# Kernel tuning notes

Hardware: AMD Instinct MI355X
Metric: run time of the kernel (lower is better)

Reference implementation:

```python
import jax, jax.numpy as jnp
import numpy as np

N_NODES = 100000
N_EDGES = 1600000
D_FEAT = 64
ORDER = 2


def setup_inputs() -> dict:
    key = jax.random.key(0)
    k1, k2, k3, k4 = jax.random.split(key, 4)
    x = jax.random.normal(k1, (N_NODES, D_FEAT), dtype=jnp.float32)
    edge_row = jnp.sort(jax.random.randint(k2, (N_EDGES,), 0, N_NODES, dtype=jnp.int32))
    edge_col = jax.random.randint(k3, (N_EDGES,), 0, N_NODES, dtype=jnp.int32)
    # positive edge weights ~ normalized adjacency values
    edge_val = jax.random.uniform(k4, (N_EDGES,), dtype=jnp.float32)
    return {"x": x, "edge_row": edge_row, "edge_col": edge_col, "edge_val": edge_val}


def reference(x, edge_row, edge_col, edge_val):
    # SGConvolution: x <- adj @ x, repeated `order` times (no trainable params).
    # adj is sparse COO: adj[edge_row[e], edge_col[e]] = edge_val[e].
    def spmm(h):
        # gather source features, scale by edge weight, scatter-add to rows
        msg = edge_val[:, None] * h[edge_col]          # [E, D]
        return jax.ops.segment_sum(msg, edge_row, num_segments=N_NODES)  # [N, D]

    h = x
    for _ in range(ORDER):
        h = spmm(h)
    return h
```

## Files before the change

kernel.cpp:

```cpp
#include <hip/hip_runtime.h>
#include <hip/hip_fp16.h>


#define N_NODES 100000
#define N_EDGES 1600000
#define D_FEAT  64
#define EPW     64
#define CH      16

__device__ __forceinline__ float readlane_f(float x, int j) {
    return __uint_as_float(__builtin_amdgcn_readlane(__float_as_uint(x), j));
}

__device__ __forceinline__ float to_f32(float x)  { return x; }
__device__ __forceinline__ float to_f32(__half x) { return __half2float(x); }

template <typename GT>
__global__ __launch_bounds__(256) void sg_spmm(
    const GT*    __restrict__ h,
    const int*   __restrict__ erow,
    const int*   __restrict__ ecol,
    const float* __restrict__ eval,
    float*       __restrict__ out)
{
    const int lane  = threadIdx.x & 63;
    const int wave  = (int)((blockIdx.x * blockDim.x + threadIdx.x) >> 6);
    const int start = wave * EPW;

    const int   r_v = erow[start + lane];
    const int   c_v = ecol[start + lane];
    const float w_v = eval[start + lane];

    GT gbuf[2][CH];

#pragma unroll
    for (int j = 0; j < CH; ++j) {
        const int c = __builtin_amdgcn_readlane(c_v, j);
        gbuf[0][j] = h[(size_t)c * D_FEAT + lane];
    }

    int   cur_row = __builtin_amdgcn_readlane(r_v, 0);
    float acc     = 0.0f;

#pragma unroll
    for (int k = 0; k < EPW / CH; ++k) {
        if (k + 1 < EPW / CH) {
#pragma unroll
            for (int j = 0; j < CH; ++j) {
                const int c = __builtin_amdgcn_readlane(c_v, (k + 1) * CH + j);
                gbuf[(k + 1) & 1][j] = h[(size_t)c * D_FEAT + lane];
            }
        }
#pragma unroll
        for (int j = 0; j < CH; ++j) {
            const int e = k * CH + j;
            const int r = __builtin_amdgcn_readlane(r_v, e);
            if (r != cur_row) {
                atomicAdd(&out[(size_t)cur_row * D_FEAT + lane], acc);
                acc = 0.0f;
                cur_row = r;
            }
            acc += readlane_f(w_v, e) * to_f32(gbuf[k & 1][j]);
        }
    }
    atomicAdd(&out[(size_t)cur_row * D_FEAT + lane], acc);
}

__global__ __launch_bounds__(256) void cast_f32_to_f16(
    const float* __restrict__ in, __half* __restrict__ out, int n4)
{
    const int i = blockIdx.x * blockDim.x + threadIdx.x;
    if (i >= n4) return;
    const float4 v = ((const float4*)in)[i];
    __half2 a = __floats2half2_rn(v.x, v.y);
    __half2 b = __floats2half2_rn(v.z, v.w);
    ((__half2*)out)[2 * i]     = a;
    ((__half2*)out)[2 * i + 1] = b;
}

extern "C" void kernel_launch(void* const* d_in, const int* in_sizes, int n_in,
                              void* d_out, int out_size, void* d_ws, size_t ws_size,
                              hipStream_t stream) {
    const float* x    = (const float*)d_in[0];
    const int*   erow = (const int*)  d_in[1];
    const int*   ecol = (const int*)  d_in[2];
    const float* eval = (const float*)d_in[3];
    float*       out  = (float*)d_out;

    const size_t n_elem     = (size_t)N_NODES * D_FEAT;
    const size_t f32_bytes  = n_elem * sizeof(float);
    const size_t f16_bytes  = n_elem * sizeof(__half);

    float*  h1f32 = (float*)d_ws;
    __half* h16   = (__half*)((char*)d_ws + f32_bytes);

    const int threads = 256;
    const int spmm_blocks = (N_EDGES / EPW) * 64 / threads;
    const int n4          = (int)(n_elem / 4);
    const int cast_blocks = (n4 + threads - 1) / threads;

    hipMemsetAsync(h1f32, 0, f32_bytes, stream);
    hipMemsetAsync(out,   0, f32_bytes, stream);

    if (ws_size >= f32_bytes + f16_bytes) {
        cast_f32_to_f16<<<cast_blocks, threads, 0, stream>>>(x, h16, n4);
        sg_spmm<__half><<<spmm_blocks, threads, 0, stream>>>(h16, erow, ecol, eval, h1f32);
        cast_f32_to_f16<<<cast_blocks, threads, 0, stream>>>(h1f32, h16, n4);
        sg_spmm<__half><<<spmm_blocks, threads, 0, stream>>>(h16, erow, ecol, eval, out);
    } else {
        sg_spmm<float><<<spmm_blocks, threads, 0, stream>>>(x, erow, ecol, eval, h1f32);
        sg_spmm<float><<<spmm_blocks, threads, 0, stream>>>(h1f32, erow, ecol, eval, out);
    }
}
```

Before: 170.1 us.

## Fuse prep into one kernel and accumulate first SpMM directly in fp16

One prep kernel now does the input cast to fp16 and zeroes both the intermediate buffer and the output, replacing two memsets and a cast launch. The first SpMM flushes its row partials as packed half2 atomics straight into an fp16 intermediate, which removes the fp32 intermediate and the second cast kernel. Atomic traffic for that stage is halved. In exchange the intermediate sum is accumulated in half precision through many atomics, so rounding error grows, and the fallback path for a small workspace is gone.

```diff
diff --git a/kernel.cpp b/kernel.cpp
--- a/kernel.cpp
+++ b/kernel.cpp
@@ -8,20 +8,37 @@
 #define EPW     64
 #define CH      16
 
+#define N_ELEM   (N_NODES * D_FEAT)
+#define N_CAST   (N_ELEM / 4)
+#define N_Z16    (N_ELEM / 8)
+#define N_ZOUT   (N_ELEM / 4)
+#define PREP_TASKS (N_CAST + N_Z16 + N_ZOUT)
+
 __device__ __forceinline__ float readlane_f(float x, int j) {
     return __uint_as_float(__builtin_amdgcn_readlane(__float_as_uint(x), j));
 }
 
-__device__ __forceinline__ float to_f32(float x)  { return x; }
-__device__ __forceinline__ float to_f32(__half x) { return __half2float(x); }
+template <bool HALF_OUT>
+__device__ __forceinline__ void flush(void* outp, int row, int lane, float acc) {
+    if constexpr (HALF_OUT) {
+        const float partner = __shfl_xor(acc, 1);
+        if ((lane & 1) == 0) {
+            __half2* o = (__half2*)outp;
+            unsafeAtomicAdd(&o[(size_t)row * (D_FEAT / 2) + (lane >> 1)],
+                            __floats2half2_rn(acc, partner));
+        }
+    } else {
+        atomicAdd(&((float*)outp)[(size_t)row * D_FEAT + lane], acc);
+    }
+}
 
-template <typename GT>
+template <bool HALF_OUT>
 __global__ __launch_bounds__(256) void sg_spmm(
-    const GT*    __restrict__ h,
-    const int*   __restrict__ erow,
-    const int*   __restrict__ ecol,
-    const float* __restrict__ eval,
-    float*       __restrict__ out)
+    const __half* __restrict__ h,
+    const int*    __restrict__ erow,
+    const int*    __restrict__ ecol,
+    const float*  __restrict__ eval,
+    void*         __restrict__ outp)
 {
     const int lane  = threadIdx.x & 63;
     const int wave  = (int)((blockIdx.x * blockDim.x + threadIdx.x) >> 6);
@@ -31,7 +48,7 @@
     const int   c_v = ecol[start + lane];
     const float w_v = eval[start + lane];
 
-    GT gbuf[2][CH];
+    __half gbuf[2][CH];
 
 #pragma unroll
     for (int j = 0; j < CH; ++j) {
@@ -56,26 +73,36 @@
             const int e = k * CH + j;
             const int r = __builtin_amdgcn_readlane(r_v, e);
             if (r != cur_row) {
-                atomicAdd(&out[(size_t)cur_row * D_FEAT + lane], acc);
+                flush<HALF_OUT>(outp, cur_row, lane, acc);
                 acc = 0.0f;
                 cur_row = r;
             }
-            acc += readlane_f(w_v, e) * to_f32(gbuf[k & 1][j]);
+            acc += readlane_f(w_v, e) * __half2float(gbuf[k & 1][j]);
         }
     }
-    atomicAdd(&out[(size_t)cur_row * D_FEAT + lane], acc);
+    flush<HALF_OUT>(outp, cur_row, lane, acc);
 }
 
-__global__ __launch_bounds__(256) void cast_f32_to_f16(
-    const float* __restrict__ in, __half* __restrict__ out, int n4)
+__global__ __launch_bounds__(256) void prep(
+    const float* __restrict__ x,
+    __half*      __restrict__ h16a,
+    __half*      __restrict__ h16b,
+    float*       __restrict__ out)
 {
     const int i = blockIdx.x * blockDim.x + threadIdx.x;
-    if (i >= n4) return;
-    const float4 v = ((const float4*)in)[i];
-    __half2 a = __floats2half2_rn(v.x, v.y);
-    __half2 b = __floats2half2_rn(v.z, v.w);
-    ((__half2*)out)[2 * i]     = a;
-    ((__half2*)out)[2 * i + 1] = b;
+    if (i < N_CAST) {
+        const float4 v = ((const float4*)x)[i];
+        const __half2 a = __floats2half2_rn(v.x, v.y);
+        const __half2 b = __floats2half2_rn(v.z, v.w);
+        uint2 u;
+        u.x = *(const unsigned int*)&a;
+        u.y = *(const unsigned int*)&b;
+        ((uint2*)h16a)[i] = u;
+    } else if (i < N_CAST + N_Z16) {
+        ((uint4*)h16b)[i - N_CAST] = make_uint4(0u, 0u, 0u, 0u);
+    } else {
+        ((float4*)out)[i - (N_CAST + N_Z16)] = make_float4(0.f, 0.f, 0.f, 0.f);
+    }
 }
 
 extern "C" void kernel_launch(void* const* d_in, const int* in_sizes, int n_in,
@@ -87,28 +114,14 @@
     const float* eval = (const float*)d_in[3];
     float*       out  = (float*)d_out;
 
-    const size_t n_elem     = (size_t)N_NODES * D_FEAT;
-    const size_t f32_bytes  = n_elem * sizeof(float);
-    const size_t f16_bytes  = n_elem * sizeof(__half);
+    __half* h16a = (__half*)d_ws;
+    __half* h16b = h16a + N_ELEM;
 
-    float*  h1f32 = (float*)d_ws;
-    __half* h16   = (__half*)((char*)d_ws + f32_bytes);
+    const int threads     = 256;
+    const int prep_blocks = PREP_TASKS / threads;
+    const int spmm_blocks = (N_EDGES / EPW) * 64 / threads;
 
-    const int threads = 256;
-    const int spmm_blocks = (N_EDGES / EPW) * 64 / threads;
-    const int n4          = (int)(n_elem / 4);
-    const int cast_blocks = (n4 + threads - 1) / threads;
-
-    hipMemsetAsync(h1f32, 0, f32_bytes, stream);
-    hipMemsetAsync(out,   0, f32_bytes, stream);
-
-    if (ws_size >= f32_bytes + f16_bytes) {
-        cast_f32_to_f16<<<cast_blocks, threads, 0, stream>>>(x, h16, n4);
-        sg_spmm<__half><<<spmm_blocks, threads, 0, stream>>>(h16, erow, ecol, eval, h1f32);
-        cast_f32_to_f16<<<cast_blocks, threads, 0, stream>>>(h1f32, h16, n4);
-        sg_spmm<__half><<<spmm_blocks, threads, 0, stream>>>(h16, erow, ecol, eval, out);
-    } else {
-        sg_spmm<float><<<spmm_blocks, threads, 0, stream>>>(x, erow, ecol, eval, h1f32);
-        sg_spmm<float><<<spmm_blocks, threads, 0, stream>>>(h1f32, erow, ecol, eval, out);
-    }
+    prep<<<prep_blocks, threads, 0, stream>>>(x, h16a, h16b, out);
+    sg_spmm<true ><<<spmm_blocks, threads, 0, stream>>>(h16a, erow, ecol, eval, h16b);
+    sg_spmm<false><<<spmm_blocks, threads, 0, stream>>>(h16b, erow, ecol, eval, out);
 }
```

Measured after the change: 153.9 us. -9.5%, faster.

## Fuse fp16 casts into SpMM by accumulating intermediate with half2 atomics

Applied to the files above, without the earlier changes.

The first SpMM pass now reads fp32 input directly and accumulates into an fp16 intermediate using packed half2 atomics. The second pass gathers that fp16 buffer and writes fp32 output. This removes both cast kernels, the fp32 intermediate buffer and one memset. In exchange, the first pass gathers fp32 rows and accumulates in fp16 atomics, which reduces precision. The output buffer is no longer zeroed before atomics accumulate into it.

```diff
diff --git a/kernel.cpp b/kernel.cpp
--- a/kernel.cpp
+++ b/kernel.cpp
@@ -8,6 +8,8 @@
 #define EPW     64
 #define CH      16
 
+#define N_ELEM  (N_NODES * D_FEAT)
+
 __device__ __forceinline__ float readlane_f(float x, int j) {
     return __uint_as_float(__builtin_amdgcn_readlane(__float_as_uint(x), j));
 }
@@ -15,13 +17,27 @@
 __device__ __forceinline__ float to_f32(float x)  { return x; }
 __device__ __forceinline__ float to_f32(__half x) { return __half2float(x); }
 
-template <typename GT>
+template <bool HALF_OUT>
+__device__ __forceinline__ void flush(void* outp, int row, int lane, float acc) {
+    if constexpr (HALF_OUT) {
+        const float partner = __shfl_xor(acc, 1);
+        if ((lane & 1) == 0) {
+            __half2* o = (__half2*)outp;
+            unsafeAtomicAdd(&o[(size_t)row * (D_FEAT / 2) + (lane >> 1)],
+                            __floats2half2_rn(acc, partner));
+        }
+    } else {
+        atomicAdd(&((float*)outp)[(size_t)row * D_FEAT + lane], acc);
+    }
+}
+
+template <typename GT, bool HALF_OUT>
 __global__ __launch_bounds__(256) void sg_spmm(
     const GT*    __restrict__ h,
     const int*   __restrict__ erow,
     const int*   __restrict__ ecol,
     const float* __restrict__ eval,
-    float*       __restrict__ out)
+    void*        __restrict__ outp)
 {
     const int lane  = threadIdx.x & 63;
     const int wave  = (int)((blockIdx.x * blockDim.x + threadIdx.x) >> 6);
@@ -56,26 +72,14 @@
             const int e = k * CH + j;
             const int r = __builtin_amdgcn_readlane(r_v, e);
             if (r != cur_row) {
-                atomicAdd(&out[(size_t)cur_row * D_FEAT + lane], acc);
+                flush<HALF_OUT>(outp, cur_row, lane, acc);
                 acc = 0.0f;
                 cur_row = r;
             }
             acc += readlane_f(w_v, e) * to_f32(gbuf[k & 1][j]);
         }
     }
-    atomicAdd(&out[(size_t)cur_row * D_FEAT + lane], acc);
-}
-
-__global__ __launch_bounds__(256) void cast_f32_to_f16(
-    const float* __restrict__ in, __half* __restrict__ out, int n4)
-{
-    const int i = blockIdx.x * blockDim.x + threadIdx.x;
-    if (i >= n4) return;
-    const float4 v = ((const float4*)in)[i];
-    __half2 a = __floats2half2_rn(v.x, v.y);
-    __half2 b = __floats2half2_rn(v.z, v.w);
-    ((__half2*)out)[2 * i]     = a;
-    ((__half2*)out)[2 * i + 1] = b;
+    flush<HALF_OUT>(outp, cur_row, lane, acc);
 }
 
 extern "C" void kernel_launch(void* const* d_in, const int* in_sizes, int n_in,
@@ -87,28 +91,13 @@
     const float* eval = (const float*)d_in[3];
     float*       out  = (float*)d_out;
 
-    const size_t n_elem     = (size_t)N_NODES * D_FEAT;
-    const size_t f32_bytes  = n_elem * sizeof(float);
-    const size_t f16_bytes  = n_elem * sizeof(__half);
+    __half* h16b = (__half*)d_ws;
+    const size_t f16_bytes = (size_t)N_ELEM * sizeof(__half);
 
-    float*  h1f32 = (float*)d_ws;
-    __half* h16   = (__half*)((char*)d_ws + f32_bytes);
+    const int threads     = 256;
+    const int spmm_blocks = (N_EDGES / EPW) * 64 / threads;
 
-    const int threads = 256;
-    const int spmm_blocks = (N_EDGES / EPW) * 64 / threads;
-    const int n4          = (int)(n_elem / 4);
-    const int cast_blocks = (n4 + threads - 1) / threads;
-
-    hipMemsetAsync(h1f32, 0, f32_bytes, stream);
-    hipMemsetAsync(out,   0, f32_bytes, stream);
-
-    if (ws_size >= f32_bytes + f16_bytes) {
-        cast_f32_to_f16<<<cast_blocks, threads, 0, stream>>>(x, h16, n4);
-        sg_spmm<__half><<<spmm_blocks, threads, 0, stream>>>(h16, erow, ecol, eval, h1f32);
-        cast_f32_to_f16<<<cast_blocks, threads, 0, stream>>>(h1f32, h16, n4);
-        sg_spmm<__half><<<spmm_blocks, threads, 0, stream>>>(h16, erow, ecol, eval, out);
-    } else {
-        sg_spmm<float><<<spmm_blocks, threads, 0, stream>>>(x, erow, ecol, eval, h1f32);
-        sg_spmm<float><<<spmm_blocks, threads, 0, stream>>>(h1f32, erow, ecol, eval, out);
-    }
+    hipMemsetAsync(h16b, 0, f16_bytes, stream);
+    sg_spmm<float,  true ><<<spmm_blocks, threads, 0, stream>>>(x,    erow, ecol, eval, h16b);
+    sg_spmm<__half, false><<<spmm_blocks, threads, 0, stream>>>(h16b, erow, ecol, eval, out);
 }
```

New measurement: 170.2 us. No clear change (+0.1%).
